# Optimization experiments

Measured on AMD Instinct MI355X. Metric: run time of the kernel, lower is better.

## Reference

```python
import jax, jax.numpy as jnp
import numpy as np

B, S, E, H = 2, 2048, 2048, 16
NOPE, ROPE, VD = 128, 64, 128
QH = NOPE + ROPE  # 192
LORA = 512
ROPE_THETA = 10000.0
EPS = 1e-6


def setup_inputs() -> dict:
    key = jax.random.key(0)
    ks = jax.random.split(key, 5)
    sd = lambda n: 1.0 / np.sqrt(n)
    return {
        "x": jax.random.normal(ks[0], (B, S, E), jnp.float32),
        "wq": jax.random.normal(ks[1], (E, H * QH), jnp.float32) * sd(E),
        "wkv_a": jax.random.normal(ks[2], (E, LORA + ROPE), jnp.float32) * sd(E),
        "wkv_b": jax.random.normal(ks[3], (LORA, H * (NOPE + VD)), jnp.float32) * sd(LORA),
        "wo": jax.random.normal(ks[4], (H * VD, E), jnp.float32) * sd(H * VD),
        "kv_norm_scale": jnp.ones((LORA,), jnp.float32),
    }


def _rope(xp, cos, sin):
    # xp: (..., s, d); cos/sin: (s, d//2)
    d2 = xp.shape[-1] // 2
    x1, x2 = xp[..., :d2], xp[..., d2:]
    return jnp.concatenate([x1 * cos - x2 * sin, x2 * cos + x1 * sin], axis=-1)


def reference(x, wq, wkv_a, wkv_b, wo, kv_norm_scale):
    b, s, _ = x.shape
    # queries: (b, H, s, QH), split into no-pe / pe slices
    q = (x @ wq).reshape(b, s, H, QH).transpose(0, 2, 1, 3)
    q_nope, q_pe = q[..., :NOPE], q[..., NOPE:]

    # low-rank KV latent projection
    kva = x @ wkv_a  # (b, s, LORA + ROPE)
    ckv, k_pe = kva[..., :LORA], kva[..., LORA:]
    ckv = ckv * jax.lax.rsqrt(jnp.mean(ckv * ckv, axis=-1, keepdims=True) + EPS)
    ckv = ckv * kv_norm_scale  # RMSNorm on latent
    kv = (ckv @ wkv_b).reshape(b, s, H, NOPE + VD).transpose(0, 2, 1, 3)
    k_nope, v = kv[..., :NOPE], kv[..., NOPE:]

    # partial RoPE on the rope slice only
    pos = jnp.arange(s, dtype=jnp.float32)
    inv = 1.0 / (ROPE_THETA ** (jnp.arange(0, ROPE, 2, dtype=jnp.float32) / ROPE))
    ang = pos[:, None] * inv  # (s, ROPE//2)
    cos, sin = jnp.cos(ang), jnp.sin(ang)
    q_pe = _rope(q_pe, cos, sin)                 # (b, H, s, ROPE)
    k_pe = _rope(k_pe[:, None, :, :], cos, sin)  # (b, 1, s, ROPE), shared over heads

    # concat (the new_empty + slice-write in torch)
    qs = jnp.concatenate([q_nope, q_pe], axis=-1)  # (b, H, s, QH)
    ks_ = jnp.concatenate(
        [k_nope, jnp.broadcast_to(k_pe, (b, H, s, ROPE))], axis=-1
    )  # (b, H, s, QH)

    # causal SDPA with scale = q_head_dim**-0.5; asymmetric V head dim
    scale = QH ** -0.5
    scores = jnp.einsum('bhqd,bhkd->bhqk', qs, ks_) * scale
    causal = jnp.tril(jnp.ones((s, s), dtype=bool))
    scores = jnp.where(causal, scores, jnp.finfo(scores.dtype).min)
    attn = jax.nn.softmax(scores, axis=-1)
    out = jnp.einsum('bhqk,bhkd->bhqd', attn, v)  # (b, H, s, VD)
    out = out.transpose(0, 2, 1, 3).reshape(b, s, H * VD)
    return out @ wo
```

## Files before the change

kernel.cpp:

```cpp
#include <hip/hip_runtime.h>
#include <stdint.h>
#include <stddef.h>

typedef __bf16 bf16x8 __attribute__((ext_vector_type(8)));
typedef float floatx4 __attribute__((ext_vector_type(4)));
typedef unsigned short u16;

__device__ __forceinline__ float bf2f(u16 h) {
    unsigned u = ((unsigned)h) << 16;
    return __builtin_bit_cast(float, u);
}
__device__ __forceinline__ u16 f2bf(float f) {
    unsigned u = __builtin_bit_cast(unsigned, f);
    u += 0x7fffu + ((u >> 16) & 1u);
    return (u16)(u >> 16);
}

__device__ __forceinline__ void gload16(const void* g, void* l) {
    __builtin_amdgcn_global_load_lds(
        (const __attribute__((address_space(1))) uint32_t*)g,
        (__attribute__((address_space(3))) uint32_t*)l, 16, 0, 0);
}

__device__ __forceinline__ void wait_vm8() { asm volatile("s_waitcnt vmcnt(8)" ::: "memory"); }
__device__ __forceinline__ void wait_vm6() { asm volatile("s_waitcnt vmcnt(6)" ::: "memory"); }
__device__ __forceinline__ void wait_vm4() { asm volatile("s_waitcnt vmcnt(4)" ::: "memory"); }
__device__ __forceinline__ void wait_vm3() { asm volatile("s_waitcnt vmcnt(3)" ::: "memory"); }
__device__ __forceinline__ void wait_vm0() { asm volatile("s_waitcnt vmcnt(0)" ::: "memory"); }

__global__ __launch_bounds__(256) void k_conv_x(const float* __restrict__ in,
                                                u16* __restrict__ out, int n8) {
    int i = blockIdx.x * 256 + threadIdx.x;
    if (i >= n8) return;
    const float* f = in + (size_t)i * 8;
    unsigned o[4];
    for (int t = 0; t < 4; t++) {
        u16 lo = f2bf(f[2 * t]), hi = f2bf(f[2 * t + 1]);
        o[t] = (unsigned)lo | ((unsigned)hi << 16);
    }
    uint4 p = {o[0], o[1], o[2], o[3]};
    *(uint4*)&out[(size_t)i * 8] = p;
}

__global__ __launch_bounds__(256) void k_convT(const float* __restrict__ in,
                                               u16* __restrict__ out, int K, int N) {
    __shared__ u16 t[32][33];
    int k0 = blockIdx.x * 32, n0 = blockIdx.y * 32;
    int c = threadIdx.x & 31, r8 = threadIdx.x >> 5;
    for (int j = 0; j < 4; j++) {
        int row = r8 + j * 8;
        int n = n0 + c;
        t[row][c] = (n < N) ? f2bf(in[(size_t)(k0 + row) * N + n]) : (u16)0;
    }
    __syncthreads();
    for (int j = 0; j < 4; j++) {
        int row = r8 + j * 8;
        out[(size_t)(n0 + row) * K + k0 + c] = t[c][row];
    }
}

template <int NWC, int MODE>
__global__ __launch_bounds__(512, 2) void k_gemm256(const u16* __restrict__ A,
                                                    const u16* __restrict__ BT,
                                                    void* __restrict__ C0,
                                                    void* __restrict__ C1,
                                                    int K, int ldc) {
    constexpr int MFR = 16 / (8 / NWC);
    constexpr int ACH = 2;
    constexpr int BCH = NWC / 2;
    constexpr int SLOT = 8192 + NWC * 2048;
    __shared__ __align__(16) u16 RING[4][SLOT];
    int tid = threadIdx.x;
    int w = tid >> 6, lane = tid & 63;
    int l15 = lane & 15, quad = lane >> 4;
    int wr = w / NWC, wc = w % NWC;

    int gx = gridDim.x;
    int nwg = gx * gridDim.y;
    int flat = blockIdx.y * gx + blockIdx.x;
    int cpx = nwg >> 3;
    int swz = (flat & 7) * cpx + (flat >> 3);
    int bx = swz % gx, by = swz / gx;
    size_t m0 = (size_t)bx * 256, n0 = (size_t)by * (NWC * 64);
    int NT = K >> 5;

    const u16* srcA[ACH];
    const u16* srcB[BCH];
    int ldsAb[ACH], ldsBb[BCH];
#pragma unroll
    for (int p = 0; p < ACH; p++) {
        int chunk = p * 512 + tid;
        int s = chunk >> 6;
        int b = (chunk & 63) * 8;
        int bu = b ^ (((b >> 8) & 1) << 4);
        int r = bu >> 5, c = bu & 31;
        srcA[p] = A + (m0 + s * 16 + r) * (size_t)K + c;
        ldsAb[p] = (p * 512 + w * 64) * 8;
    }
#pragma unroll
    for (int p = 0; p < BCH; p++) {
        int chunk = p * 512 + tid;
        int s = chunk >> 6;
        int b = (chunk & 63) * 8;
        int bu = b ^ (((b >> 8) & 1) << 4);
        int r = bu >> 5, c = bu & 31;
        srcB[p] = BT + (n0 + s * 16 + r) * (size_t)K + c;
        ldsBb[p] = 8192 + (p * 512 + w * 64) * 8;
    }

    const int swb = (l15 * 32 + quad * 8) ^ ((l15 >> 3) << 4);

    floatx4 acc[MFR][4];
    const floatx4 fzero = {0.f, 0.f, 0.f, 0.f};
#pragma unroll
    for (int i = 0; i < MFR; i++)
#pragma unroll
        for (int j = 0; j < 4; j++) acc[i][j] = fzero;

    bf16x8 aA0[MFR], bB0[4], aA1[MFR], bB1[4];

    auto STAGE = [&](int j) {
        int rs = j & 3;
        size_t ko = (size_t)j * 32;
        u16* ring = &RING[rs][0];
#pragma unroll
        for (int p = 0; p < ACH; p++) gload16(srcA[p] + ko, ring + ldsAb[p]);
#pragma unroll
        for (int p = 0; p < BCH; p++) gload16(srcB[p] + ko, ring + ldsBb[p]);
    };
    auto READ0 = [&](int rs) {
        const u16* ring = &RING[rs][0];
#pragma unroll
        for (int i2 = 0; i2 < MFR; i2++)
            aA0[i2] = *(const bf16x8*)&ring[(wr * MFR + i2) * 512 + swb];
#pragma unroll
        for (int j2 = 0; j2 < 4; j2++)
            bB0[j2] = *(const bf16x8*)&ring[8192 + (wc * 4 + j2) * 512 + swb];
    };
    auto READ1 = [&](int rs) {
        const u16* ring = &RING[rs][0];
#pragma unroll
        for (int i2 = 0; i2 < MFR; i2++)
            aA1[i2] = *(const bf16x8*)&ring[(wr * MFR + i2) * 512 + swb];
#pragma unroll
        for (int j2 = 0; j2 < 4; j2++)
            bB1[j2] = *(const bf16x8*)&ring[8192 + (wc * 4 + j2) * 512 + swb];
    };
    auto MMA0 = [&]() {
#pragma unroll
        for (int i2 = 0; i2 < MFR; i2++)
#pragma unroll
            for (int j2 = 0; j2 < 4; j2++)
                acc[i2][j2] = __builtin_amdgcn_mfma_f32_16x16x32_bf16(
                    aA0[i2], bB0[j2], acc[i2][j2], 0, 0, 0);
    };
    auto MMA1 = [&]() {
#pragma unroll
        for (int i2 = 0; i2 < MFR; i2++)
#pragma unroll
            for (int j2 = 0; j2 < 4; j2++)
                acc[i2][j2] = __builtin_amdgcn_mfma_f32_16x16x32_bf16(
                    aA1[i2], bB1[j2], acc[i2][j2], 0, 0, 0);
    };

    STAGE(0); STAGE(1); STAGE(2);

    if constexpr (NWC == 4) {
        int j = 0;
        for (; j + 3 < NT; j++) {
            wait_vm8();
            __builtin_amdgcn_s_barrier();
            __builtin_amdgcn_sched_barrier(0);
            READ0(j & 3);
            STAGE(j + 3);
            __builtin_amdgcn_sched_barrier(0);
            MMA0();
        }
        {
            wait_vm8();
            __builtin_amdgcn_s_barrier();
            __builtin_amdgcn_sched_barrier(0);
            READ0(j & 3); MMA0(); j++;
        }
        {
            wait_vm4();
            __builtin_amdgcn_s_barrier();
            __builtin_amdgcn_sched_barrier(0);
            READ0(j & 3); MMA0(); j++;
        }
        {
            wait_vm0();
            __builtin_amdgcn_s_barrier();
            __builtin_amdgcn_sched_barrier(0);
            READ0(j & 3); MMA0();
        }
    } else {
        wait_vm6();
        __builtin_amdgcn_s_barrier();
        __builtin_amdgcn_sched_barrier(0);
        READ0(0);
        for (int j = 0; j + 1 < NT; j += 2) {
            if (j + 2 < NT) wait_vm3(); else wait_vm0();
            __builtin_amdgcn_s_barrier();
            __builtin_amdgcn_sched_barrier(0);
            READ1((j + 1) & 3);
            if (j + 3 < NT) STAGE(j + 3);
            MMA0();
            if (j + 2 < NT) {
                if (j + 3 < NT) wait_vm3(); else wait_vm0();
                __builtin_amdgcn_s_barrier();
                __builtin_amdgcn_sched_barrier(0);
                READ0((j + 2) & 3);
                if (j + 4 < NT) STAGE(j + 4);
            }
            MMA1();
        }
    }

#pragma unroll
    for (int i = 0; i < MFR; i++)
#pragma unroll
        for (int j2 = 0; j2 < 4; j2++) {
            size_t col = n0 + wc * 64 + j2 * 16 + l15;
#pragma unroll
            for (int r = 0; r < 4; r++) {
                size_t row = m0 + (size_t)wr * (MFR * 16) + i * 16 + quad * 4 + r;
                if constexpr (MODE == 0) {
                    ((u16*)C0)[row * ldc + col] = f2bf(acc[i][j2][r]);
                } else if constexpr (MODE == 1) {
                    ((float*)C0)[row * ldc + col] = acc[i][j2][r];
                } else if constexpr (MODE == 2) {
                    if (col < 3072)
                        ((u16*)C0)[row * 3072 + col] = f2bf(acc[i][j2][r]);
                    else if (col < 3648)
                        ((u16*)C1)[row * 576 + (col - 3072)] = f2bf(acc[i][j2][r]);
                }
            }
            if constexpr (MODE == 3) {
                int cm = (int)(col & 255);
                size_t row0 = m0 + (size_t)wr * (MFR * 16) + i * 16 + quad * 4;
                if (cm < 128) {
#pragma unroll
                    for (int r = 0; r < 4; r++)
                        ((u16*)C0)[(row0 + r) * 4096 + col] = f2bf(acc[i][j2][r]);
                } else {
                    int h = (int)(col >> 8), vd = cm - 128;
                    size_t b = row0 >> 11, s = row0 & 2047;
                    unsigned lo = (unsigned)f2bf(acc[i][j2][0]) | ((unsigned)f2bf(acc[i][j2][1]) << 16);
                    unsigned hi = (unsigned)f2bf(acc[i][j2][2]) | ((unsigned)f2bf(acc[i][j2][3]) << 16);
                    uint2 pk = {lo, hi};
                    *(uint2*)&((u16*)C1)[(((b << 4) + h) * 128 + vd) * 2048 + s] = pk;
                }
            }
        }
}

__global__ __launch_bounds__(64) void k_rmsnorm(const u16* __restrict__ kva,
                                                const float* __restrict__ scl,
                                                u16* __restrict__ ckv) {
    int r = blockIdx.x, lane = threadIdx.x;
    const u16* row = kva + (size_t)r * 576 + lane * 8;
    uint4 raw = *(const uint4*)row;
    unsigned w[4] = {raw.x, raw.y, raw.z, raw.w};
    float f[8];
    float ss = 0.f;
    for (int t = 0; t < 4; t++) {
        f[2 * t]     = bf2f((u16)(w[t] & 0xffffu));
        f[2 * t + 1] = bf2f((u16)(w[t] >> 16));
        ss += f[2 * t] * f[2 * t] + f[2 * t + 1] * f[2 * t + 1];
    }
    for (int off = 1; off < 64; off <<= 1) ss += __shfl_xor(ss, off, 64);
    float rs = rsqrtf(ss * (1.f / 512.f) + 1e-6f);
    unsigned o[4];
    for (int t = 0; t < 4; t++) {
        u16 lo = f2bf(f[2 * t] * rs * scl[lane * 8 + 2 * t]);
        u16 hi = f2bf(f[2 * t + 1] * rs * scl[lane * 8 + 2 * t + 1]);
        o[t] = (unsigned)lo | ((unsigned)hi << 16);
    }
    uint4 packed = {o[0], o[1], o[2], o[3]};
    *(uint4*)(ckv + (size_t)r * 512 + lane * 8) = packed;
}

__global__ __launch_bounds__(256) void k_rope(u16* __restrict__ qbuf, u16* __restrict__ kva) {
    int tid = threadIdx.x;
    int rloc = tid >> 7;
    int task = tid & 127;
    int r = blockIdx.x * 2 + rloc;
    __shared__ float cs_s[2][32], sn_s[2][32];
    if (tid < 64) {
        int rr = tid >> 5, i = tid & 31;
        int ss = (blockIdx.x * 2 + rr) & 2047;
        float freq = __expf(-0.28782313662425575f * (float)i);
        float ang = (float)ss * freq;
        float sn, cs;
        sincosf(ang, &sn, &cs);
        cs_s[rr][i] = cs; sn_s[rr][i] = sn;
    }
    __syncthreads();
    if (task < 68) {
        int rb = task >> 2, q = task & 3;
        u16* base = (rb < 16) ? qbuf + (size_t)r * 3072 + rb * 192 + 128
                              : kva + (size_t)r * 576 + 512;
        u16* p1 = base + q * 8;
        uint4 x1v = *(uint4*)p1;
        uint4 x2v = *(uint4*)(p1 + 32);
        unsigned w1[4] = {x1v.x, x1v.y, x1v.z, x1v.w};
        unsigned w2[4] = {x2v.x, x2v.y, x2v.z, x2v.w};
        unsigned o1[4], o2[4];
        for (int t2 = 0; t2 < 4; t2++) {
            float a1 = bf2f((u16)(w1[t2] & 0xffffu)), b1 = bf2f((u16)(w1[t2] >> 16));
            float a2 = bf2f((u16)(w2[t2] & 0xffffu)), b2 = bf2f((u16)(w2[t2] >> 16));
            int i0 = q * 8 + t2 * 2, i1 = i0 + 1;
            float c0 = cs_s[rloc][i0], s0 = sn_s[rloc][i0];
            float c1 = cs_s[rloc][i1], s1 = sn_s[rloc][i1];
            o1[t2] = (unsigned)f2bf(a1 * c0 - a2 * s0) | ((unsigned)f2bf(b1 * c1 - b2 * s1) << 16);
            o2[t2] = (unsigned)f2bf(a2 * c0 + a1 * s0) | ((unsigned)f2bf(b2 * c1 + b1 * s1) << 16);
        }
        uint4 y1 = {o1[0], o1[1], o1[2], o1[3]};
        uint4 y2 = {o2[0], o2[1], o2[2], o2[3]};
        *(uint4*)p1 = y1;
        *(uint4*)(p1 + 32) = y2;
    }
}

__global__ __launch_bounds__(256, 3) void k_attn(const u16* __restrict__ qbuf,
                                                 const u16* __restrict__ kv,
                                                 const u16* __restrict__ kva,
                                                 const u16* __restrict__ vt,
                                                 u16* __restrict__ attno) {
    int tid = threadIdx.x;
    int wave = tid >> 6, lane = tid & 63;
    int quad = lane >> 4, l15 = lane & 15;
    int hb = blockIdx.x;
    int h = hb & 15, b = hb >> 4;
    int qb = 31 - (int)blockIdx.y;
    int qg0 = qb * 64 + wave * 16;
    int row = qg0 + l15;

    __shared__ __align__(16) u16 Kn[2][32 * 136];
    __shared__ __align__(16) u16 Kp[2][32 * 72];
    __shared__ __align__(16) u16 Vs[2][128 * 40];
    __shared__ __align__(16) u16 P[4][16 * 40];

    const u16* qrp = qbuf + ((size_t)(b * 2048) + qg0 + l15) * 3072 + h * 192;
    bf16x8 qf[6];
    for (int c = 0; c < 6; c++) qf[c] = *(const bf16x8*)&qrp[c * 32 + quad * 8];

    const floatx4 fzero = {0.f, 0.f, 0.f, 0.f};
    floatx4 o[8];
    for (int f = 0; f < 8; f++) o[f] = fzero;
    float lp = 0.f;

    const u16* kvb = kv  + (size_t)(b * 2048) * 4096 + h * 256;
    const u16* kpb = kva + (size_t)(b * 2048) * 576 + 512;
    const u16* vtb = vt  + (size_t)(b * 16 + h) * 128 * 2048;
    const float scale = 0.07216878364870323f;

    int nkt = qb * 2 + 2;

    int kKey0 = tid >> 4,          kOff0 = (tid & 15) * 8;
    int kKey1 = (tid + 256) >> 4,  kOff1 = (tid & 15) * 8;
    int pKey  = tid >> 3,          pOff  = (tid & 7) * 8;
    int vRow0 = tid >> 2,          vOff0 = (tid & 3) * 8;
    int vRow1 = (tid + 256) >> 2,  vOff1 = (tid & 3) * 8;

    {
        uint4 a = *(const uint4*)&kvb[(size_t)kKey0 * 4096 + kOff0];
        uint4 c = *(const uint4*)&kvb[(size_t)kKey1 * 4096 + kOff1];
        uint4 d = *(const uint4*)&kpb[(size_t)pKey * 576 + pOff];
        uint4 e = *(const uint4*)&vtb[(size_t)vRow0 * 2048 + vOff0];
        uint4 g = *(const uint4*)&vtb[(size_t)vRow1 * 2048 + vOff1];
        *(uint4*)&Kn[0][kKey0 * 136 + kOff0] = a;
        *(uint4*)&Kn[0][kKey1 * 136 + kOff1] = c;
        *(uint4*)&Kp[0][pKey * 72 + pOff] = d;
        *(uint4*)&Vs[0][vRow0 * 40 + vOff0] = e;
        *(uint4*)&Vs[0][vRow1 * 40 + vOff1] = g;
    }
    __syncthreads();

    for (int kt = 0; kt < nkt; kt++) {
        int cur = kt & 1;
        bool have = (kt + 1) < nkt;
        uint4 sA = {}, sB = {}, sC = {}, sD = {}, sE = {};
        if (have) {
            int kb = (kt + 1) * 32;
            sA = *(const uint4*)&kvb[(size_t)(kb + kKey0) * 4096 + kOff0];
            sB = *(const uint4*)&kvb[(size_t)(kb + kKey1) * 4096 + kOff1];
            sC = *(const uint4*)&kpb[(size_t)(kb + pKey) * 576 + pOff];
            sD = *(const uint4*)&vtb[(size_t)vRow0 * 2048 + kb + vOff0];
            sE = *(const uint4*)&vtb[(size_t)vRow1 * 2048 + kb + vOff1];
        }
        if (kt * 32 <= qg0 + 15) {
            bf16x8 vf[8];
            for (int f = 0; f < 8; f++)
                vf[f] = *(const bf16x8*)&Vs[cur][(f * 16 + l15) * 40 + quad * 8];
            floatx4 sc[2] = {fzero, fzero};
            for (int hf = 0; hf < 2; hf++) {
                const u16* kn = &Kn[cur][(hf * 16 + l15) * 136];
                const u16* kp = &Kp[cur][(hf * 16 + l15) * 72];
                for (int c = 0; c < 4; c++) {
                    bf16x8 kf = *(const bf16x8*)&kn[c * 32 + quad * 8];
                    sc[hf] = __builtin_amdgcn_mfma_f32_16x16x32_bf16(kf, qf[c], sc[hf], 0, 0, 0);
                }
                for (int c = 0; c < 2; c++) {
                    bf16x8 kf = *(const bf16x8*)&kp[c * 32 + quad * 8];
                    sc[hf] = __builtin_amdgcn_mfma_f32_16x16x32_bf16(kf, qf[4 + c], sc[hf], 0, 0, 0);
                }
            }
            asm volatile("" ::: "memory");
            for (int hf = 0; hf < 2; hf++) {
                int keyb = kt * 32 + hf * 16 + quad * 4;
                float p[4];
                for (int r = 0; r < 4; r++)
                    p[r] = (keyb + r <= row) ? __expf(sc[hf][r] * scale) : 0.f;
                lp += (p[0] + p[1]) + (p[2] + p[3]);
                unsigned d0 = (unsigned)f2bf(p[0]) | ((unsigned)f2bf(p[1]) << 16);
                unsigned d1 = (unsigned)f2bf(p[2]) | ((unsigned)f2bf(p[3]) << 16);
                uint2 pk = {d0, d1};
                *(uint2*)&P[wave][l15 * 40 + hf * 16 + quad * 4] = pk;
            }
            asm volatile("" ::: "memory");
            bf16x8 pa = *(const bf16x8*)&P[wave][l15 * 40 + quad * 8];
            asm volatile("" ::: "memory");
            for (int f = 0; f < 8; f++)
                o[f] = __builtin_amdgcn_mfma_f32_16x16x32_bf16(pa, vf[f], o[f], 0, 0, 0);
        }
        if (have) {
            int nb = cur ^ 1;
            *(uint4*)&Kn[nb][kKey0 * 136 + kOff0] = sA;
            *(uint4*)&Kn[nb][kKey1 * 136 + kOff1] = sB;
            *(uint4*)&Kp[nb][pKey * 72 + pOff] = sC;
            *(uint4*)&Vs[nb][vRow0 * 40 + vOff0] = sD;
            *(uint4*)&Vs[nb][vRow1 * 40 + vOff1] = sE;
        }
        __syncthreads();
    }

    lp += __shfl_xor(lp, 16, 64);
    lp += __shfl_xor(lp, 32, 64);
    float lrow[4];
    for (int r = 0; r < 4; r++) lrow[r] = __shfl(lp, quad * 4 + r, 64);
    for (int f = 0; f < 8; f++)
        for (int r = 0; r < 4; r++) {
            int orow = qg0 + quad * 4 + r;
            float val = o[f][r] / lrow[r];
            attno[((size_t)(b * 2048) + orow) * 2048 + h * 128 + f * 16 + l15] = f2bf(val);
        }
}

extern "C" void kernel_launch(void* const* d_in, const int* in_sizes, int n_in,
                              void* d_out, int out_size, void* d_ws, size_t ws_size,
                              hipStream_t stream) {
    const float* x_raw    = (const float*)d_in[0];
    const float* wq_raw   = (const float*)d_in[1];
    const float* wkva_raw = (const float*)d_in[2];
    const float* wkvb_raw = (const float*)d_in[3];
    const float* wo_raw   = (const float*)d_in[4];
    const float* kvs_raw  = (const float*)d_in[5];
    float* out = (float*)d_out;
    u16* ws = (u16*)d_ws;

    const size_t O_ATT = 0;
    const size_t O_VT  = 8388608;
    const size_t O_QB  = 16777216;
    const size_t O_KVA = 29360128;
    const size_t O_KV  = 31719424;
    const size_t TOTAL_BYTES = 48496640ull * 2;
    if (ws_size < TOTAL_BYTES) return;

    u16* g12bt  = ws + O_ATT;
    u16* ckv    = ws + O_ATT;
    u16* wkvb_t = ws + O_ATT + 2097152;
    u16* attno  = ws + O_ATT;
    u16* x_bf   = ws + O_VT;
    u16* vt     = ws + O_VT;
    u16* qbuf   = ws + O_QB;
    u16* wo_t   = ws + O_QB;
    u16* kva    = ws + O_KVA;
    u16* kv     = ws + O_KV;

    k_conv_x<<<4096, 256, 0, stream>>>(x_raw, x_bf, 1048576);
    k_convT<<<dim3(64, 96), 256, 0, stream>>>(wq_raw, g12bt, 2048, 3072);
    k_convT<<<dim3(64, 24), 256, 0, stream>>>(wkva_raw, g12bt + (size_t)3072 * 2048, 2048, 576);

    k_gemm256<4, 2><<<dim3(16, 15), 512, 0, stream>>>(x_bf, g12bt, qbuf, kva, 2048, 0);

    k_rmsnorm<<<4096, 64, 0, stream>>>(kva, kvs_raw, ckv);
    k_convT<<<dim3(16, 128), 256, 0, stream>>>(wkvb_raw, wkvb_t, 512, 4096);
    k_gemm256<4, 3><<<dim3(16, 16), 512, 0, stream>>>(ckv, wkvb_t, kv, vt, 512, 4096);

    k_rope<<<2048, 256, 0, stream>>>(qbuf, kva);

    k_attn<<<dim3(32, 32), 256, 0, stream>>>(qbuf, kv, kva, vt, attno);

    k_convT<<<dim3(64, 64), 256, 0, stream>>>(wo_raw, wo_t, 2048, 2048);
    k_gemm256<2, 1><<<dim3(16, 16), 512, 0, stream>>>(attno, wo_t, out, nullptr, 2048, 2048);
}
```

Before: 354.1 us.

## Fuse RoPE into QKV GEMM epilogue and defer PV MMA in attention

```diff
diff --git a/kernel.cpp b/kernel.cpp
--- a/kernel.cpp
+++ b/kernel.cpp
@@ -214,6 +214,32 @@
                 if (j + 4 < NT) STAGE(j + 4);
             }
             MMA1();
+        }
+    }
+
+    if constexpr (MODE == 2) {
+        int colbase = (int)(n0) + wc * 64;
+        bool ropeW = ((colbase % 192) == 128) && (colbase < 3072 || colbase == 3584);
+        if (ropeW) {
+            float fq0 = __expf(-0.28782313662425575f * (float)l15);
+            float fq1 = __expf(-0.28782313662425575f * (float)(16 + l15));
+#pragma unroll
+            for (int i = 0; i < MFR; i++)
+#pragma unroll
+                for (int j2lo = 0; j2lo < 2; j2lo++) {
+                    float fq = j2lo ? fq1 : fq0;
+#pragma unroll
+                    for (int r = 0; r < 4; r++) {
+                        size_t row = m0 + (size_t)wr * (MFR * 16) + i * 16 + quad * 4 + r;
+                        int s = (int)(row & 2047);
+                        float ang = (float)s * fq;
+                        float sn, cs;
+                        sincosf(ang, &sn, &cs);
+                        float x1 = acc[i][j2lo][r], x2 = acc[i][j2lo + 2][r];
+                        acc[i][j2lo][r]     = x1 * cs - x2 * sn;
+                        acc[i][j2lo + 2][r] = x2 * cs + x1 * sn;
+                    }
+                }
         }
     }
 
@@ -281,48 +307,6 @@
     *(uint4*)(ckv + (size_t)r * 512 + lane * 8) = packed;
 }
 
-__global__ __launch_bounds__(256) void k_rope(u16* __restrict__ qbuf, u16* __restrict__ kva) {
-    int tid = threadIdx.x;
-    int rloc = tid >> 7;
-    int task = tid & 127;
-    int r = blockIdx.x * 2 + rloc;
-    __shared__ float cs_s[2][32], sn_s[2][32];
-    if (tid < 64) {
-        int rr = tid >> 5, i = tid & 31;
-        int ss = (blockIdx.x * 2 + rr) & 2047;
-        float freq = __expf(-0.28782313662425575f * (float)i);
-        float ang = (float)ss * freq;
-        float sn, cs;
-        sincosf(ang, &sn, &cs);
-        cs_s[rr][i] = cs; sn_s[rr][i] = sn;
-    }
-    __syncthreads();
-    if (task < 68) {
-        int rb = task >> 2, q = task & 3;
-        u16* base = (rb < 16) ? qbuf + (size_t)r * 3072 + rb * 192 + 128
-                              : kva + (size_t)r * 576 + 512;
-        u16* p1 = base + q * 8;
-        uint4 x1v = *(uint4*)p1;
-        uint4 x2v = *(uint4*)(p1 + 32);
-        unsigned w1[4] = {x1v.x, x1v.y, x1v.z, x1v.w};
-        unsigned w2[4] = {x2v.x, x2v.y, x2v.z, x2v.w};
-        unsigned o1[4], o2[4];
-        for (int t2 = 0; t2 < 4; t2++) {
-            float a1 = bf2f((u16)(w1[t2] & 0xffffu)), b1 = bf2f((u16)(w1[t2] >> 16));
-            float a2 = bf2f((u16)(w2[t2] & 0xffffu)), b2 = bf2f((u16)(w2[t2] >> 16));
-            int i0 = q * 8 + t2 * 2, i1 = i0 + 1;
-            float c0 = cs_s[rloc][i0], s0 = sn_s[rloc][i0];
-            float c1 = cs_s[rloc][i1], s1 = sn_s[rloc][i1];
-            o1[t2] = (unsigned)f2bf(a1 * c0 - a2 * s0) | ((unsigned)f2bf(b1 * c1 - b2 * s1) << 16);
-            o2[t2] = (unsigned)f2bf(a2 * c0 + a1 * s0) | ((unsigned)f2bf(b2 * c1 + b1 * s1) << 16);
-        }
-        uint4 y1 = {o1[0], o1[1], o1[2], o1[3]};
-        uint4 y2 = {o2[0], o2[1], o2[2], o2[3]};
-        *(uint4*)p1 = y1;
-        *(uint4*)(p1 + 32) = y2;
-    }
-}
-
 __global__ __launch_bounds__(256, 3) void k_attn(const u16* __restrict__ qbuf,
                                                  const u16* __restrict__ kv,
                                                  const u16* __restrict__ kva,
@@ -350,6 +334,7 @@
     floatx4 o[8];
     for (int f = 0; f < 8; f++) o[f] = fzero;
     float lp = 0.f;
+    bf16x8 vfp[8];
 
     const u16* kvb = kv  + (size_t)(b * 2048) * 4096 + h * 256;
     const u16* kpb = kva + (size_t)(b * 2048) * 576 + 512;
@@ -390,10 +375,14 @@
             sD = *(const uint4*)&vtb[(size_t)vRow0 * 2048 + kb + vOff0];
             sE = *(const uint4*)&vtb[(size_t)vRow1 * 2048 + kb + vOff1];
         }
+        if (kt > 0 && (kt - 1) * 32 <= qg0 + 15) {
+            bf16x8 pa = *(const bf16x8*)&P[wave][l15 * 40 + quad * 8];
+            for (int f = 0; f < 8; f++)
+                o[f] = __builtin_amdgcn_mfma_f32_16x16x32_bf16(pa, vfp[f], o[f], 0, 0, 0);
+        }
         if (kt * 32 <= qg0 + 15) {
-            bf16x8 vf[8];
             for (int f = 0; f < 8; f++)
-                vf[f] = *(const bf16x8*)&Vs[cur][(f * 16 + l15) * 40 + quad * 8];
+                vfp[f] = *(const bf16x8*)&Vs[cur][(f * 16 + l15) * 40 + quad * 8];
             floatx4 sc[2] = {fzero, fzero};
             for (int hf = 0; hf < 2; hf++) {
                 const u16* kn = &Kn[cur][(hf * 16 + l15) * 136];
@@ -420,10 +409,6 @@
                 *(uint2*)&P[wave][l15 * 40 + hf * 16 + quad * 4] = pk;
             }
             asm volatile("" ::: "memory");
-            bf16x8 pa = *(const bf16x8*)&P[wave][l15 * 40 + quad * 8];
-            asm volatile("" ::: "memory");
-            for (int f = 0; f < 8; f++)
-                o[f] = __builtin_amdgcn_mfma_f32_16x16x32_bf16(pa, vf[f], o[f], 0, 0, 0);
         }
         if (have) {
             int nb = cur ^ 1;
@@ -434,6 +419,11 @@
             *(uint4*)&Vs[nb][vRow1 * 40 + vOff1] = sE;
         }
         __syncthreads();
+    }
+    if ((nkt - 1) * 32 <= qg0 + 15) {
+        bf16x8 pa = *(const bf16x8*)&P[wave][l15 * 40 + quad * 8];
+        for (int f = 0; f < 8; f++)
+            o[f] = __builtin_amdgcn_mfma_f32_16x16x32_bf16(pa, vfp[f], o[f], 0, 0, 0);
     }
 
     lp += __shfl_xor(lp, 16, 64);
@@ -489,8 +479,6 @@
     k_convT<<<dim3(16, 128), 256, 0, stream>>>(wkvb_raw, wkvb_t, 512, 4096);
     k_gemm256<4, 3><<<dim3(16, 16), 512, 0, stream>>>(ckv, wkvb_t, kv, vt, 512, 4096);
 
-    k_rope<<<2048, 256, 0, stream>>>(qbuf, kva);
-
     k_attn<<<dim3(32, 32), 256, 0, stream>>>(qbuf, kv, kva, vt, attno);
 
     k_convT<<<dim3(64, 64), 256, 0, stream>>>(wo_raw, wo_t, 2048, 2048);
```

After: 495.3 us. 1.4x slower.
